# Performance work log

Hardware: AMD Instinct MI355X
Metric: run time of the kernel (lower is better)

## Reference

```python
import jax, jax.numpy as jnp
import numpy as np

EPS = 1e-6
BLK = 16  # NVFP4 block size (16 elements share one e4m3 scale)
# e2m1 representable magnitudes and rounding midpoints
GRID = jnp.array([0.0, 0.5, 1.0, 1.5, 2.0, 3.0, 4.0, 6.0], dtype=jnp.float32)
MID = jnp.array([0.25, 0.75, 1.25, 1.75, 2.5, 3.5, 5.0], dtype=jnp.float32)


def _e2m1(x):
    # round magnitude to nearest e2m1 grid point (saturate at 6.0)
    a = jnp.minimum(jnp.abs(x), 6.0)
    idx = jnp.searchsorted(MID, a, side='right')
    return jnp.sign(x) * jnp.take(GRID, idx)


def _fp4_quant_scaled(x, gscale):
    # vllm scaled_fp4_quant: per-16 block amax -> e4m3 block scale (scaled by
    # global scale), quantize to e2m1. Returns q * s8 (= dequant * gscale).
    m, n = x.shape
    xb = x.reshape(m, n // BLK, BLK)
    amax = jnp.max(jnp.abs(xb), axis=-1, keepdims=True)
    s8 = (amax * gscale / 6.0).astype(jnp.float8_e4m3fn).astype(jnp.float32)
    safe = jnp.where(s8 > 0, s8, 1.0)
    q = _e2m1(jnp.where(s8 > 0, xb * gscale / safe, 0.0))
    return (q * s8).reshape(m, n)


def _fp4_mm(y, w, ag, wg):
    # cutlass_scaled_fp4_mm with alpha = 1/(ag*wg): dequantized matmul y @ w.T
    alpha = 1.0 / (ag * wg)
    yq = _fp4_quant_scaled(y, ag)   # [m, h]
    wq = _fp4_quant_scaled(w, wg)   # [h, h]
    return (yq @ wq.T) * alpha


def _rmsnorm(x, w):
    v = jnp.mean(x * x, axis=-1, keepdims=True)
    return x * jax.lax.rsqrt(v + EPS) * w


def setup_inputs() -> dict:
    key = jax.random.key(0)
    k1, k2, k3, k4 = jax.random.split(key, 4)
    T, H = 8192, 4096
    hidden_states = jax.random.normal(k1, (T, H), dtype=jnp.float32)
    norm_w = jnp.ones((4, H), dtype=jnp.float32)          # RMSNorm weights (init ones)
    w = jax.random.uniform(k2, (3, H, H), dtype=jnp.float32)     # torch.rand
    agscale = jax.random.uniform(k3, (3,), dtype=jnp.float32, minval=0.25, maxval=1.0)
    wgscale = jax.random.uniform(k4, (3,), dtype=jnp.float32, minval=0.25, maxval=1.0)
    return {"hidden_states": hidden_states, "norm_w": norm_w, "w": w,
            "agscale": agscale, "wgscale": wgscale}


def reference(hidden_states, norm_w, w, agscale, wgscale):
    # tensor_model_parallel_all_reduce == identity on a single device
    x = jnp.maximum(hidden_states, 0.0)  # relu
    resid = x
    y = _rmsnorm(x, norm_w[0])
    for i in range(3):  # 3 structurally distinct layers (fixed small loop)
        z = _fp4_mm(y, w[i], agscale[i], wgscale[i])
        resid = z + resid                # fused add
        y = _rmsnorm(resid, norm_w[i + 1])
    return y
```

## Files before the change

### kernel.cpp

```cpp
#include <hip/hip_runtime.h>
#include <stdint.h>

#define HD 4096
#define TD 8192

typedef unsigned short u16;
typedef unsigned int u32;
typedef __bf16 bf16x8 __attribute__((ext_vector_type(8)));
typedef float f32x4 __attribute__((ext_vector_type(4)));

#define GL16(gp, lp) __builtin_amdgcn_global_load_lds( \
    (__attribute__((address_space(1))) void*)(void*)(uintptr_t)(gp), \
    (__attribute__((address_space(3))) void*)(lp), 16, 0, 0)


__device__ __forceinline__ float e4m3_rtne(float f) {
  if (f <= 0.0f) return 0.0f;
  unsigned u = __float_as_uint(f);
  int e = (int)((u >> 23) & 0xff) - 127;
  if (e < -6) e = -6;
  float C = __uint_as_float((unsigned)(e + 147) << 23);
  float r = (f + C) - C;
  return fminf(r, 448.0f);
}

__device__ __forceinline__ void quant_store16(const float v[16], float g, u16* dst) {
  float amax = 0.0f;
#pragma unroll
  for (int j = 0; j < 16; ++j) amax = fmaxf(amax, fabsf(v[j]));
  float s = e4m3_rtne(amax * g / 6.0f);
  u32 out[8];
  if (s > 0.0f) {
    const float m1 = 0.25f * s, m2 = 0.75f * s, m3 = 1.25f * s, m4 = 1.75f * s;
    const float m5 = 2.5f * s, m6 = 3.5f * s, m7 = 5.0f * s;
#pragma unroll
    for (int p = 0; p < 8; ++p) {
      u16 b[2];
#pragma unroll
      for (int h = 0; h < 2; ++h) {
        float t = v[2 * p + h] * g;
        float u = fabsf(t);
        float q = (u < m4) ? ((u < m2) ? ((u < m1) ? 0.0f : 0.5f)
                                       : ((u < m3) ? 1.0f : 1.5f))
                           : ((u < m6) ? ((u < m5) ? 2.0f : 3.0f)
                                       : ((u < m7) ? 4.0f : 6.0f));
        float val = copysignf(q * s, t);
        b[h] = (u16)(__float_as_uint(val) >> 16);
      }
      out[p] = (u32)b[0] | ((u32)b[1] << 16);
    }
  } else {
#pragma unroll
    for (int p = 0; p < 8; ++p) out[p] = 0u;
  }
  uint4* d4 = (uint4*)dst;
  d4[0] = make_uint4(out[0], out[1], out[2], out[3]);
  d4[1] = make_uint4(out[4], out[5], out[6], out[7]);
}

__device__ __forceinline__ float block_sum256(float v) {
#pragma unroll
  for (int off = 32; off > 0; off >>= 1) v += __shfl_down(v, off, 64);
  __shared__ float red[4];
  int tid = threadIdx.x;
  if ((tid & 63) == 0) red[tid >> 6] = v;
  __syncthreads();
  return (red[0] + red[1]) + (red[2] + red[3]);
}


__global__ __launch_bounds__(256) void k_relu_norm_quant(
    const float* __restrict__ hs, const float* __restrict__ nw,
    const float* __restrict__ agp, float* __restrict__ resid,
    u16* __restrict__ yq) {
  const int row = blockIdx.x, tid = threadIdx.x;
  const size_t base = (size_t)row * HD + tid * 16;
  float v[16];
#pragma unroll
  for (int j = 0; j < 4; ++j) ((float4*)v)[j] = ((const float4*)(hs + base))[j];
  float ss = 0.0f;
#pragma unroll
  for (int j = 0; j < 16; ++j) {
    v[j] = fmaxf(v[j], 0.0f);
    ss += v[j] * v[j];
  }
#pragma unroll
  for (int j = 0; j < 4; ++j) ((float4*)(resid + base))[j] = ((float4*)v)[j];
  float tot = block_sum256(ss);
  float rs = 1.0f / sqrtf(tot * (1.0f / HD) + 1e-6f);
  const float* nwp = nw + tid * 16;
  float y[16];
#pragma unroll
  for (int j = 0; j < 16; ++j) y[j] = v[j] * rs * nwp[j];
  quant_store16(y, agp[0], yq + base);
}

__global__ __launch_bounds__(256) void k_norm_quant(
    const float* __restrict__ resid, const float* __restrict__ nw,
    const float* __restrict__ agp, int li, u16* __restrict__ yq) {
  const int row = blockIdx.x, tid = threadIdx.x;
  const size_t base = (size_t)row * HD + tid * 16;
  float v[16];
#pragma unroll
  for (int j = 0; j < 4; ++j) ((float4*)v)[j] = ((const float4*)(resid + base))[j];
  float ss = 0.0f;
#pragma unroll
  for (int j = 0; j < 16; ++j) ss += v[j] * v[j];
  float tot = block_sum256(ss);
  float rs = 1.0f / sqrtf(tot * (1.0f / HD) + 1e-6f);
  const float* nwp = nw + (size_t)li * HD + tid * 16;
  float y[16];
#pragma unroll
  for (int j = 0; j < 16; ++j) y[j] = v[j] * rs * nwp[j];
  quant_store16(y, agp[li], yq + base);
}

__global__ __launch_bounds__(256) void k_final_norm(
    float* __restrict__ io, const float* __restrict__ nw) {
  const int row = blockIdx.x, tid = threadIdx.x;
  const size_t base = (size_t)row * HD + tid * 16;
  float v[16];
#pragma unroll
  for (int j = 0; j < 4; ++j) ((float4*)v)[j] = ((const float4*)(io + base))[j];
  float ss = 0.0f;
#pragma unroll
  for (int j = 0; j < 16; ++j) ss += v[j] * v[j];
  float tot = block_sum256(ss);
  float rs = 1.0f / sqrtf(tot * (1.0f / HD) + 1e-6f);
  const float* nwp = nw + (size_t)3 * HD + tid * 16;
#pragma unroll
  for (int j = 0; j < 16; ++j) v[j] = v[j] * rs * nwp[j];
#pragma unroll
  for (int j = 0; j < 4; ++j) ((float4*)(io + base))[j] = ((float4*)v)[j];
}

__global__ __launch_bounds__(256) void k_quant_w(
    const float* __restrict__ w, const float* __restrict__ wgp, int li,
    u16* __restrict__ wq) {
  const int row = blockIdx.x, tid = threadIdx.x;
  const size_t base = (size_t)li * HD * HD + (size_t)row * HD + tid * 16;
  float v[16];
#pragma unroll
  for (int j = 0; j < 4; ++j) ((float4*)v)[j] = ((const float4*)(w + base))[j];
  quant_store16(v, wgp[li], wq + (size_t)row * HD + tid * 16);
}


#define BARF() do { asm volatile("" ::: "memory"); \
    __builtin_amdgcn_s_barrier(); \
    asm volatile("" ::: "memory"); } while (0)
#define WLG() asm volatile("s_waitcnt lgkmcnt(0)" ::: "memory")
#define WVM6() asm volatile("s_waitcnt vmcnt(6)" ::: "memory")

__global__ __launch_bounds__(512, 2) void k_gemm(
    const u16* __restrict__ A, const u16* __restrict__ B,
    float* __restrict__ resid, const float* __restrict__ agp,
    const float* __restrict__ wgp, int layer) {
  __shared__ __align__(16) u16 ldsA[2 * 256 * 64];
  __shared__ __align__(16) u16 ldsB[2 * 256 * 64];
  const int tid = threadIdx.x;
  const int lane = tid & 63, wave = tid >> 6;
  const int wr = wave >> 2, wc = wave & 3;
  const int r = lane & 15, q = lane >> 4;

  int bid = blockIdx.x;
  bid = (bid & 7) * 64 + (bid >> 3);
  const int m0 = (bid >> 4) * 256;
  const int n0 = (bid & 15) * 256;

  const int rs = tid >> 3;
  const int cs = ((tid & 7) ^ (rs & 7)) * 8;
  const u16* gA = A + (size_t)(m0 + rs) * HD + cs;
  const u16* gB = B + (size_t)(n0 + rs) * HD + cs;
  u16* lA = ldsA + tid * 8;
  u16* lB = ldsB + tid * 8;

#define STG_A(bb, h, koff) do { \
    GL16(gA + (size_t)(h) * (128 * HD) + (koff), lA + (bb) + (h) * 8192); \
    GL16(gA + (size_t)(h) * (128 * HD) + 64 * HD + (koff), lA + (bb) + (h) * 8192 + 4096); \
  } while (0)
#define STG_B(bb, h, koff) do { \
    GL16(gB + (size_t)(h) * (128 * HD) + (koff), lB + (bb) + (h) * 8192); \
    GL16(gB + (size_t)(h) * (128 * HD) + 64 * HD + (koff), lB + (bb) + (h) * 8192 + 4096); \
  } while (0)

  const int sa = (q ^ (r & 7)) * 8;
  const int sb = ((q + 4) ^ (r & 7)) * 8;
  const int arow = (wr * 128 + r) * 64;
  const int brow = (wc * 64 + r) * 64;

  f32x4 acc[8][4];
#pragma unroll
  for (int i = 0; i < 8; ++i)
#pragma unroll
    for (int j = 0; j < 4; ++j) acc[i][j] = (f32x4){0.f, 0.f, 0.f, 0.f};

  bf16x8 a[4][2], b[4][2];

#define LD_A(base) do { \
    _Pragma("unroll") \
    for (int mi = 0; mi < 4; ++mi) { \
      a[mi][0] = *(const bf16x8*)((base) + arow + mi * 1024 + sa); \
      a[mi][1] = *(const bf16x8*)((base) + arow + mi * 1024 + sb); \
    } } while (0)
#define LD_B(base) do { \
    _Pragma("unroll") \
    for (int nj = 0; nj < 4; ++nj) { \
      b[nj][0] = *(const bf16x8*)((base) + brow + nj * 1024 + sa); \
      b[nj][1] = *(const bf16x8*)((base) + brow + nj * 1024 + sb); \
    } } while (0)
#define MMQ(mh, nh) do { \
    _Pragma("unroll") \
    for (int mi = 0; mi < 4; ++mi) \
    _Pragma("unroll") \
    for (int nj = 0; nj < 2; ++nj) { \
      acc[(mh) * 4 + mi][(nh) * 2 + nj] = __builtin_amdgcn_mfma_f32_16x16x32_bf16( \
          a[mi][0], b[(nh) * 2 + nj][0], acc[(mh) * 4 + mi][(nh) * 2 + nj], 0, 0, 0); \
      acc[(mh) * 4 + mi][(nh) * 2 + nj] = __builtin_amdgcn_mfma_f32_16x16x32_bf16( \
          a[mi][1], b[(nh) * 2 + nj][1], acc[(mh) * 4 + mi][(nh) * 2 + nj], 0, 0, 0); \
    } } while (0)

  STG_B(0, 0, 0); STG_B(0, 1, 0);
  STG_A(0, 0, 0); STG_A(0, 1, 0);
  STG_B(16384, 0, 64); STG_B(16384, 1, 64);
  STG_A(16384, 0, 64);
  WVM6();
  BARF();

  for (int i = 0; i < 32; ++i) {
    const int kb = i * 128;
    const int k1 = kb + 64;
    int k2 = kb + 128; if (k2 >= HD) k2 -= HD;
    int k3 = kb + 192; if (k3 >= HD) k3 -= HD;
    LD_A(ldsA); LD_B(ldsB);
    STG_A(16384, 1, k1);
    BARF(); WLG();
    __builtin_amdgcn_s_setprio(1); MMQ(0, 0); __builtin_amdgcn_s_setprio(0);
    BARF();
    STG_B(0, 0, k2);
    BARF();
    __builtin_amdgcn_s_setprio(1); MMQ(0, 1); __builtin_amdgcn_s_setprio(0);
    BARF();
    LD_A(ldsA + 4096);
    STG_B(0, 1, k2);
    BARF(); WLG();
    __builtin_amdgcn_s_setprio(1); MMQ(1, 0); __builtin_amdgcn_s_setprio(0);
    BARF();
    STG_A(0, 0, k2);
    WVM6();
    BARF();
    __builtin_amdgcn_s_setprio(1); MMQ(1, 1); __builtin_amdgcn_s_setprio(0);
    BARF();
    LD_A(ldsA + 16384); LD_B(ldsB + 16384);
    STG_A(0, 1, k2);
    BARF(); WLG();
    __builtin_amdgcn_s_setprio(1); MMQ(0, 0); __builtin_amdgcn_s_setprio(0);
    BARF();
    STG_B(16384, 0, k3);
    BARF();
    __builtin_amdgcn_s_setprio(1); MMQ(0, 1); __builtin_amdgcn_s_setprio(0);
    BARF();
    LD_A(ldsA + 16384 + 4096);
    STG_B(16384, 1, k3);
    BARF(); WLG();
    __builtin_amdgcn_s_setprio(1); MMQ(1, 0); __builtin_amdgcn_s_setprio(0);
    BARF();
    STG_A(16384, 0, k3);
    WVM6();
    BARF();
    __builtin_amdgcn_s_setprio(1); MMQ(1, 1); __builtin_amdgcn_s_setprio(0);
    BARF();
  }

  const float alpha = 1.0f / (agp[layer] * wgp[layer]);
#pragma unroll
  for (int mi = 0; mi < 8; ++mi) {
    const int gm0 = m0 + wr * 128 + mi * 16 + q * 4;
#pragma unroll
    for (int nj = 0; nj < 4; ++nj) {
      const int gn = n0 + wc * 64 + nj * 16 + r;
#pragma unroll
      for (int t = 0; t < 4; ++t) {
        float* p = resid + (size_t)(gm0 + t) * HD + gn;
        *p = fmaf(acc[mi][nj][t], alpha, *p);
      }
    }
  }
}


extern "C" void kernel_launch(void* const* d_in, const int* in_sizes, int n_in,
                              void* d_out, int out_size, void* d_ws, size_t ws_size,
                              hipStream_t stream) {
  const float* hs = (const float*)d_in[0];
  const float* nw = (const float*)d_in[1];
  const float* w = (const float*)d_in[2];
  const float* ag = (const float*)d_in[3];
  const float* wg = (const float*)d_in[4];
  float* out = (float*)d_out;

  u16* wq = (u16*)d_ws;
  u16* yq = (u16*)d_ws + (size_t)HD * HD;

  k_relu_norm_quant<<<TD, 256, 0, stream>>>(hs, nw, ag, out, yq);
  for (int l = 0; l < 3; ++l) {
    k_quant_w<<<HD, 256, 0, stream>>>(w, wg, l, wq);
    k_gemm<<<dim3((TD / 256) * (HD / 256)), 512, 0, stream>>>(yq, wq, out, ag, wg, l);
    if (l < 2) k_norm_quant<<<TD, 256, 0, stream>>>(out, nw, ag, l + 1, yq);
  }
  k_final_norm<<<TD, 256, 0, stream>>>(out, nw);
}
```

Measured before the change: 1.325 ms.

## Switch GEMM to 32x32x16 MFMA, stage epilogue through LDS, batch weight quant

The GEMM inner loop now uses 32x32x16 bf16 MFMA tiles with f32x16 accumulators in place of 16x16x32. Operands are loaded with a matching swizzled layout. The epilogue writes accumulators to LDS in two halves and then does coalesced float4 read-modify-write of the residual, replacing scattered scalar updates. When the workspace is large enough, all three weight matrices are quantized in one kernel launch instead of three. Costs are extra LDS round-trips and barriers in the epilogue, a larger workspace requirement, and register-pressure changes from the bigger MFMA accumulators.

```diff
diff --git a/kernel.cpp b/kernel.cpp
--- a/kernel.cpp
+++ b/kernel.cpp
@@ -8,6 +8,7 @@
 typedef unsigned int u32;
 typedef __bf16 bf16x8 __attribute__((ext_vector_type(8)));
 typedef float f32x4 __attribute__((ext_vector_type(4)));
+typedef float f32x16 __attribute__((ext_vector_type(16)));
 
 #define GL16(gp, lp) __builtin_amdgcn_global_load_lds( \
     (__attribute__((address_space(1))) void*)(void*)(uintptr_t)(gp), \
@@ -145,6 +146,17 @@
   quant_store16(v, wgp[li], wq + (size_t)row * HD + tid * 16);
 }
 
+__global__ __launch_bounds__(256) void k_quant_w_all(
+    const float* __restrict__ w, const float* __restrict__ wgp,
+    u16* __restrict__ wq3) {
+  const int row = blockIdx.x, tid = threadIdx.x;
+  const size_t base = (size_t)row * HD + tid * 16;
+  float v[16];
+#pragma unroll
+  for (int j = 0; j < 4; ++j) ((float4*)v)[j] = ((const float4*)(w + base))[j];
+  quant_store16(v, wgp[row >> 12], wq3 + base);
+}
+
 
 #define BARF() do { asm volatile("" ::: "memory"); \
     __builtin_amdgcn_s_barrier(); \
@@ -161,7 +173,7 @@
   const int tid = threadIdx.x;
   const int lane = tid & 63, wave = tid >> 6;
   const int wr = wave >> 2, wc = wave & 3;
-  const int r = lane & 15, q = lane >> 4;
+  const int l31 = lane & 31, l5 = lane >> 5, l7 = lane & 7;
 
   int bid = blockIdx.x;
   bid = (bid & 7) * 64 + (bid >> 3);
@@ -184,40 +196,43 @@
     GL16(gB + (size_t)(h) * (128 * HD) + 64 * HD + (koff), lB + (bb) + (h) * 8192 + 4096); \
   } while (0)
 
-  const int sa = (q ^ (r & 7)) * 8;
-  const int sb = ((q + 4) ^ (r & 7)) * 8;
-  const int arow = (wr * 128 + r) * 64;
-  const int brow = (wc * 64 + r) * 64;
-
-  f32x4 acc[8][4];
-#pragma unroll
-  for (int i = 0; i < 8; ++i)
-#pragma unroll
-    for (int j = 0; j < 4; ++j) acc[i][j] = (f32x4){0.f, 0.f, 0.f, 0.f};
-
-  bf16x8 a[4][2], b[4][2];
-
-#define LD_A(base) do { \
-    _Pragma("unroll") \
-    for (int mi = 0; mi < 4; ++mi) { \
-      a[mi][0] = *(const bf16x8*)((base) + arow + mi * 1024 + sa); \
-      a[mi][1] = *(const bf16x8*)((base) + arow + mi * 1024 + sb); \
-    } } while (0)
-#define LD_B(base) do { \
-    _Pragma("unroll") \
-    for (int nj = 0; nj < 4; ++nj) { \
-      b[nj][0] = *(const bf16x8*)((base) + brow + nj * 1024 + sa); \
-      b[nj][1] = *(const bf16x8*)((base) + brow + nj * 1024 + sb); \
-    } } while (0)
-#define MMQ(mh, nh) do { \
-    _Pragma("unroll") \
-    for (int mi = 0; mi < 4; ++mi) \
-    _Pragma("unroll") \
-    for (int nj = 0; nj < 2; ++nj) { \
-      acc[(mh) * 4 + mi][(nh) * 2 + nj] = __builtin_amdgcn_mfma_f32_16x16x32_bf16( \
-          a[mi][0], b[(nh) * 2 + nj][0], acc[(mh) * 4 + mi][(nh) * 2 + nj], 0, 0, 0); \
-      acc[(mh) * 4 + mi][(nh) * 2 + nj] = __builtin_amdgcn_mfma_f32_16x16x32_bf16( \
-          a[mi][1], b[(nh) * 2 + nj][1], acc[(mh) * 4 + mi][(nh) * 2 + nj], 0, 0, 0); \
+  const int wm = wr * 128, wn = wc * 64;
+  const int aoff = (wm + l31) * 64;
+  const int boff = (wn + l31) * 64;
+  const int ck[4] = {((0 + l5) ^ l7) * 8, ((2 + l5) ^ l7) * 8,
+                     ((4 + l5) ^ l7) * 8, ((6 + l5) ^ l7) * 8};
+
+  f32x16 acc[4][2];
+#pragma unroll
+  for (int i = 0; i < 4; ++i)
+#pragma unroll
+    for (int j = 0; j < 2; ++j)
+#pragma unroll
+      for (int p = 0; p < 16; ++p) acc[i][j][p] = 0.0f;
+
+  bf16x8 a[2][4], b[2][4];
+
+#define LD_A32(base, mh) do { \
+    _Pragma("unroll") \
+    for (int mi = 0; mi < 2; ++mi) \
+    _Pragma("unroll") \
+    for (int ks = 0; ks < 4; ++ks) \
+      a[mi][ks] = *(const bf16x8*)((base) + aoff + ((mh) * 2 + mi) * 2048 + ck[ks]); \
+  } while (0)
+#define LD_B32(base) do { \
+    _Pragma("unroll") \
+    for (int nj = 0; nj < 2; ++nj) \
+    _Pragma("unroll") \
+    for (int ks = 0; ks < 4; ++ks) \
+      b[nj][ks] = *(const bf16x8*)((base) + boff + nj * 2048 + ck[ks]); \
+  } while (0)
+#define MMQ32(mh, nh) do { \
+    _Pragma("unroll") \
+    for (int ks = 0; ks < 4; ++ks) { \
+      acc[(mh) * 2 + 0][nh] = __builtin_amdgcn_mfma_f32_32x32x16_bf16( \
+          a[0][ks], b[nh][ks], acc[(mh) * 2 + 0][nh], 0, 0, 0); \
+      acc[(mh) * 2 + 1][nh] = __builtin_amdgcn_mfma_f32_32x32x16_bf16( \
+          a[1][ks], b[nh][ks], acc[(mh) * 2 + 1][nh], 0, 0, 0); \
     } } while (0)
 
   STG_B(0, 0, 0); STG_B(0, 1, 0);
@@ -232,59 +247,87 @@
     const int k1 = kb + 64;
     int k2 = kb + 128; if (k2 >= HD) k2 -= HD;
     int k3 = kb + 192; if (k3 >= HD) k3 -= HD;
-    LD_A(ldsA); LD_B(ldsB);
+    LD_A32(ldsA, 0); LD_B32(ldsB);
     STG_A(16384, 1, k1);
     BARF(); WLG();
-    __builtin_amdgcn_s_setprio(1); MMQ(0, 0); __builtin_amdgcn_s_setprio(0);
+    __builtin_amdgcn_s_setprio(1); MMQ32(0, 0); __builtin_amdgcn_s_setprio(0);
     BARF();
     STG_B(0, 0, k2);
     BARF();
-    __builtin_amdgcn_s_setprio(1); MMQ(0, 1); __builtin_amdgcn_s_setprio(0);
-    BARF();
-    LD_A(ldsA + 4096);
+    __builtin_amdgcn_s_setprio(1); MMQ32(0, 1); __builtin_amdgcn_s_setprio(0);
+    BARF();
+    LD_A32(ldsA, 1);
     STG_B(0, 1, k2);
     BARF(); WLG();
-    __builtin_amdgcn_s_setprio(1); MMQ(1, 0); __builtin_amdgcn_s_setprio(0);
+    __builtin_amdgcn_s_setprio(1); MMQ32(1, 0); __builtin_amdgcn_s_setprio(0);
     BARF();
     STG_A(0, 0, k2);
     WVM6();
     BARF();
-    __builtin_amdgcn_s_setprio(1); MMQ(1, 1); __builtin_amdgcn_s_setprio(0);
-    BARF();
-    LD_A(ldsA + 16384); LD_B(ldsB + 16384);
+    __builtin_amdgcn_s_setprio(1); MMQ32(1, 1); __builtin_amdgcn_s_setprio(0);
+    BARF();
+    LD_A32(ldsA + 16384, 0); LD_B32(ldsB + 16384);
     STG_A(0, 1, k2);
     BARF(); WLG();
-    __builtin_amdgcn_s_setprio(1); MMQ(0, 0); __builtin_amdgcn_s_setprio(0);
+    __builtin_amdgcn_s_setprio(1); MMQ32(0, 0); __builtin_amdgcn_s_setprio(0);
     BARF();
     STG_B(16384, 0, k3);
     BARF();
-    __builtin_amdgcn_s_setprio(1); MMQ(0, 1); __builtin_amdgcn_s_setprio(0);
-    BARF();
-    LD_A(ldsA + 16384 + 4096);
+    __builtin_amdgcn_s_setprio(1); MMQ32(0, 1); __builtin_amdgcn_s_setprio(0);
+    BARF();
+    LD_A32(ldsA + 16384, 1);
     STG_B(16384, 1, k3);
     BARF(); WLG();
-    __builtin_amdgcn_s_setprio(1); MMQ(1, 0); __builtin_amdgcn_s_setprio(0);
+    __builtin_amdgcn_s_setprio(1); MMQ32(1, 0); __builtin_amdgcn_s_setprio(0);
     BARF();
     STG_A(16384, 0, k3);
     WVM6();
     BARF();
-    __builtin_amdgcn_s_setprio(1); MMQ(1, 1); __builtin_amdgcn_s_setprio(0);
-    BARF();
-  }
+    __builtin_amdgcn_s_setprio(1); MMQ32(1, 1); __builtin_amdgcn_s_setprio(0);
+    BARF();
+  }
+
+  asm volatile("s_waitcnt vmcnt(0)" ::: "memory");
+  __syncthreads();
 
   const float alpha = 1.0f / (agp[layer] * wgp[layer]);
-#pragma unroll
-  for (int mi = 0; mi < 8; ++mi) {
-    const int gm0 = m0 + wr * 128 + mi * 16 + q * 4;
-#pragma unroll
-    for (int nj = 0; nj < 4; ++nj) {
-      const int gn = n0 + wc * 64 + nj * 16 + r;
-#pragma unroll
-      for (int t = 0; t < 4; ++t) {
-        float* p = resid + (size_t)(gm0 + t) * HD + gn;
-        *p = fmaf(acc[mi][nj][t], alpha, *p);
+  float* const fA = (float*)ldsA;
+  float* const fB = (float*)ldsB;
+#pragma unroll
+  for (int h = 0; h < 2; ++h) {
+    if (wr == h) {
+#pragma unroll
+      for (int mt = 0; mt < 4; ++mt) {
+        float* const f = (mt < 2) ? fA : fB;
+        const int rb = (mt & 1) * 32;
+#pragma unroll
+        for (int nj = 0; nj < 2; ++nj) {
+          const int col = wn + nj * 32 + l31;
+#pragma unroll
+          for (int p = 0; p < 16; ++p) {
+            const int rowp = rb + (p & 3) + 8 * (p >> 2) + 4 * l5;
+            f[rowp * 256 + col] = acc[mt][nj][p];
+          }
+        }
       }
     }
+    __syncthreads();
+#pragma unroll
+    for (int p = 0; p < 16; ++p) {
+      const float* const f = (p < 8) ? fA : fB;
+      const int idx = (p & 7) * 512 + tid;
+      const int lrow = (p < 8 ? 0 : 64) + (idx >> 6);
+      const int c4 = idx & 63;
+      f32x4 v = *(const f32x4*)&f[(idx >> 6) * 256 + c4 * 4];
+      float4* gp = (float4*)(resid + (size_t)(m0 + h * 128 + lrow) * HD + n0) + c4;
+      float4 o = *gp;
+      o.x = fmaf(v[0], alpha, o.x);
+      o.y = fmaf(v[1], alpha, o.y);
+      o.z = fmaf(v[2], alpha, o.z);
+      o.w = fmaf(v[3], alpha, o.w);
+      *gp = o;
+    }
+    if (h == 0) __syncthreads();
   }
 }
 
@@ -299,14 +342,26 @@
   const float* wg = (const float*)d_in[4];
   float* out = (float*)d_out;
 
-  u16* wq = (u16*)d_ws;
-  u16* yq = (u16*)d_ws + (size_t)HD * HD;
-
-  k_relu_norm_quant<<<TD, 256, 0, stream>>>(hs, nw, ag, out, yq);
-  for (int l = 0; l < 3; ++l) {
-    k_quant_w<<<HD, 256, 0, stream>>>(w, wg, l, wq);
-    k_gemm<<<dim3((TD / 256) * (HD / 256)), 512, 0, stream>>>(yq, wq, out, ag, wg, l);
-    if (l < 2) k_norm_quant<<<TD, 256, 0, stream>>>(out, nw, ag, l + 1, yq);
+  const size_t need_big = ((size_t)3 * HD * HD + (size_t)TD * HD) * sizeof(u16);
+  if (ws_size >= need_big) {
+    u16* wq3 = (u16*)d_ws;
+    u16* yq = wq3 + (size_t)3 * HD * HD;
+    k_quant_w_all<<<3 * HD, 256, 0, stream>>>(w, wg, wq3);
+    k_relu_norm_quant<<<TD, 256, 0, stream>>>(hs, nw, ag, out, yq);
+    for (int l = 0; l < 3; ++l) {
+      k_gemm<<<dim3((TD / 256) * (HD / 256)), 512, 0, stream>>>(
+          yq, wq3 + (size_t)l * HD * HD, out, ag, wg, l);
+      if (l < 2) k_norm_quant<<<TD, 256, 0, stream>>>(out, nw, ag, l + 1, yq);
+    }
+  } else {
+    u16* wq = (u16*)d_ws;
+    u16* yq = (u16*)d_ws + (size_t)HD * HD;
+    k_relu_norm_quant<<<TD, 256, 0, stream>>>(hs, nw, ag, out, yq);
+    for (int l = 0; l < 3; ++l) {
+      k_quant_w<<<HD, 256, 0, stream>>>(w, wg, l, wq);
+      k_gemm<<<dim3((TD / 256) * (HD / 256)), 512, 0, stream>>>(yq, wq, out, ag, wg, l);
+      if (l < 2) k_norm_quant<<<TD, 256, 0, stream>>>(out, nw, ag, l + 1, yq);
+    }
   }
   k_final_norm<<<TD, 256, 0, stream>>>(out, nw);
 }
```

Result: slower. 1.395 ms (+5.3%).
